# Performance work log

Hardware: AMD Instinct MI355X
Metric: run time of the kernel (lower is better)

Reference implementation:

```python
import jax, jax.numpy as jnp
import numpy as np
from jax import lax

B, N, D = 4, 4096, 1024
H, DH, K = 8, 128, 256  # heads, dim_head, linformer k
KERNEL = 32
PAD = (15, 16)  # torch padding='same' for even kernel: left=(k-1)//2, right=rest


def setup_inputs() -> dict:
    key = jax.random.key(0)
    ks = jax.random.split(key, 7)
    s = 0.02
    return {
        "x": jax.random.normal(ks[0], (B, N, D), dtype=jnp.float32),
        "Wq": jax.random.normal(ks[1], (D, D), dtype=jnp.float32) * s,
        "Wk": jax.random.normal(ks[2], (D, D), dtype=jnp.float32) * s,
        "Wpk": jax.random.normal(ks[3], (K, N, KERNEL), dtype=jnp.float32) * s,
        "bpk": jax.random.normal(ks[4], (K,), dtype=jnp.float32) * s,
        "Wo": jax.random.normal(ks[5], (D, D), dtype=jnp.float32) * s,
        "bo": jax.random.normal(ks[6], (D,), dtype=jnp.float32) * s,
    }


def reference(x, Wq, Wk, Wpk, bpk, Wo, bo):
    b, n, d = x.shape
    # linear projections (torch Linear: y = x @ W.T)
    q = x @ Wq.T                       # (b, n, h*dh)
    keys = x @ Wk.T                    # (b, n, h*dh)
    # Conv1d over feature length with seq positions as channels: (b, n, d) -> (b, k, d)
    keys = lax.conv_general_dilated(
        keys, Wpk, window_strides=(1,), padding=[PAD],
        dimension_numbers=("NCH", "OIH", "NCH"),
    ) + bpk[None, :, None]             # (b, K, h*dh)
    values = keys                      # share_kv=True
    # split heads
    q = q.reshape(b, n, H, DH).transpose(0, 2, 1, 3)        # (b, h, n, dh)
    kk = keys.reshape(b, K, H, DH).transpose(0, 2, 1, 3)    # (b, h, K, dh)
    vv = values.reshape(b, K, H, DH).transpose(0, 2, 1, 3)  # (b, h, K, dh)
    dots = jnp.einsum("bhnd,bhkd->bhnk", q, kk) * (DH ** -0.5)
    attn = jax.nn.softmax(dots, axis=-1)                    # dropout p=0.0 (eval)
    out = jnp.einsum("bhnk,bhkd->bhnd", attn, vv)
    out = out.transpose(0, 2, 1, 3).reshape(b, n, H * DH)
    return out @ Wo.T + bo
```

## Files before the change

kernel.cpp:

```cpp
#include <hip/hip_runtime.h>


typedef short v8s __attribute__((ext_vector_type(8)));
typedef float v4f __attribute__((ext_vector_type(4)));

#define MFMA16(a, b, c) __builtin_amdgcn_mfma_f32_16x16x32_bf16((a), (b), (c), 0, 0, 0)
#define WAITV(N) asm volatile("s_waitcnt vmcnt(" #N ")" ::: "memory")
#define SBAR() __builtin_amdgcn_s_barrier()

__device__ __forceinline__ unsigned short f2bf(float f) {
  unsigned int u = __float_as_uint(f);
  u += 0x7fffu + ((u >> 16) & 1u);
  return (unsigned short)(u >> 16);
}

__device__ __forceinline__ v8s cvt8(float4 a, float4 b) {
  v8s v;
  v[0] = (short)f2bf(a.x); v[1] = (short)f2bf(a.y);
  v[2] = (short)f2bf(a.z); v[3] = (short)f2bf(a.w);
  v[4] = (short)f2bf(b.x); v[5] = (short)f2bf(b.y);
  v[6] = (short)f2bf(b.z); v[7] = (short)f2bf(b.w);
  return v;
}

__device__ __forceinline__ void gld16(void* lds, const void* g) {
  __builtin_amdgcn_global_load_lds(
      (const __attribute__((address_space(1))) void*)g,
      (__attribute__((address_space(3))) void*)lds, 16, 0, 0);
}

__device__ __forceinline__ const v8s* frag_ptr(const short* base, int row, int g) {
  return (const v8s*)(base + row * 32 + (((g ^ (row >> 1)) & 3) << 3));
}

__global__ __launch_bounds__(256) void k_cvt(const float* __restrict__ src,
                                             short* __restrict__ dst, int n8) {
  const int i = blockIdx.x * 256 + threadIdx.x;
  if (i >= n8) return;
  const float4* s = (const float4*)src;
  ((v8s*)dst)[i] = cvt8(s[2 * i], s[2 * i + 1]);
}

__global__ __launch_bounds__(256) void k_reorder_wpk(const float* __restrict__ Wpk,
                                                     short* __restrict__ Wr) {
  __shared__ short T[64][40];
  const int k  = blockIdx.x >> 6;
  const int n0 = (blockIdx.x & 63) << 6;
  const int tid = threadIdx.x;
  {
    const int i = tid >> 2, t0 = (tid & 3) << 3;
    const float* p = Wpk + ((size_t)k * 4096 + n0 + i) * 32 + t0;
    float4 a = *(const float4*)p, b = *(const float4*)(p + 4);
    *(v8s*)&T[i][t0] = cvt8(a, b);
  }
  __syncthreads();
  {
    const int t = tid >> 3, j0 = (tid & 7) << 3;
    v8s o;
#pragma unroll
    for (int q = 0; q < 8; ++q) o[q] = T[j0 + q][t];
    *(v8s*)(Wr + ((size_t)t * 256 + k) * 4096 + n0 + j0) = o;
  }
}

__global__ __launch_bounds__(256) void k_init_kc(const float* __restrict__ bpk,
                                                 float* __restrict__ Kc) {
  const int idx = (blockIdx.x * 256 + threadIdx.x) * 4;
  const float v = bpk[(idx >> 10) & 255];
  float4 f; f.x = v; f.y = v; f.z = v; f.w = v;
  *(float4*)(Kc + idx) = f;
}

__global__ __launch_bounds__(256) void k_zero_pad(short* __restrict__ KpTp) {
  const int idx = blockIdx.x * 256 + threadIdx.x;
  const int ridx = idx >> 9, col8 = idx & 511;
  const int b = ridx >> 5, rr = ridx & 31;
  const int row = (rr < 15) ? rr : 1039 + (rr - 15);
  v8s z = {0, 0, 0, 0, 0, 0, 0, 0};
  *(v8s*)(KpTp + ((size_t)b * 1056 + row) * 4096 + col8 * 8) = z;
}

__global__ __launch_bounds__(256) void k_gemm_qk_v3(const short* __restrict__ xbf,
                                                    const short* __restrict__ Wqk,
                                                    short* __restrict__ Qbf,
                                                    short* __restrict__ Kp) {
  __shared__ short As[2][128][32];
  __shared__ short Bs[2][128][32];
  const int tid = threadIdx.x, lane = tid & 63, w = tid >> 6;
  const int m0 = blockIdx.x * 128, j0 = blockIdx.y * 128;
  const int wr = (w >> 1) * 64, wc = (w & 1) * 64;
  const int l15 = lane & 15, g = lane >> 4;
  const int sr = lane >> 2, sseg = lane & 3;

  v4f acc[4][4];
#pragma unroll
  for (int i = 0; i < 4; ++i)
#pragma unroll
    for (int j = 0; j < 4; ++j) acc[i][j] = (v4f)0.0f;

  auto stage = [&](int buf, int k0) {
#pragma unroll
    for (int q0 = 0; q0 < 2; ++q0) {
      const int rblk = (w * 2 + q0) << 4, r = rblk + sr;
      const int co = ((sseg ^ (r >> 1)) & 3) << 3;
      gld16(&As[buf][rblk][0], xbf + (size_t)(m0 + r) * 1024 + k0 + co);
      gld16(&Bs[buf][rblk][0], Wqk + (size_t)(j0 + r) * 1024 + k0 + co);
    }
  };

  stage(0, 0);
#pragma unroll 1
  for (int p = 0, buf = 0; p < 32; ++p, buf ^= 1) {
    if (p + 1 < 32) stage(buf ^ 1, (p + 1) * 32);
    if (p < 31) { WAITV(4); } else { WAITV(0); }
    SBAR();
    v8s af[4], bf4[4];
#pragma unroll
    for (int mi = 0; mi < 4; ++mi)
      af[mi] = *frag_ptr(&As[buf][0][0], wr + mi * 16 + l15, g);
#pragma unroll
    for (int ni = 0; ni < 4; ++ni)
      bf4[ni] = *frag_ptr(&Bs[buf][0][0], wc + ni * 16 + l15, g);
#pragma unroll
    for (int ni = 0; ni < 4; ++ni)
#pragma unroll
      for (int mi = 0; mi < 4; ++mi)
        acc[mi][ni] = MFMA16(af[mi], bf4[ni], acc[mi][ni]);
    SBAR();
  }
  const int rbase = (lane >> 4) * 4;
#pragma unroll
  for (int mi = 0; mi < 4; ++mi)
#pragma unroll
    for (int ni = 0; ni < 4; ++ni) {
      const int col = j0 + wc + ni * 16 + l15;
      short* dst = (col < 1024) ? Qbf : Kp;
      const int cj = (col < 1024) ? col : col - 1024;
#pragma unroll
      for (int r = 0; r < 4; ++r) {
        const int row = m0 + wr + mi * 16 + rbase + r;
        dst[(size_t)row * 1024 + cj] = (short)f2bf(acc[mi][ni][r]);
      }
    }
}

__global__ __launch_bounds__(256) void k_transpose_pad(const short* __restrict__ src,
                                                       short* __restrict__ dst) {
  __shared__ short T[64][72];
  const int r0 = blockIdx.x * 64, c0 = blockIdx.y * 64, b = blockIdx.z;
  const int tid = threadIdx.x;
  {
    const int i = tid >> 2, q = (tid & 3) << 4;
    const short* ps = src + ((size_t)b * 4096 + r0 + i) * 1024 + c0 + q;
    *(v8s*)&T[i][q]     = *(const v8s*)ps;
    *(v8s*)&T[i][q + 8] = *(const v8s*)(ps + 8);
  }
  __syncthreads();
  {
    const int j = tid >> 2, p = (tid & 3) << 4;
    v8s o0, o1;
#pragma unroll
    for (int t = 0; t < 8; ++t) o0[t] = T[p + t][j];
#pragma unroll
    for (int t = 0; t < 8; ++t) o1[t] = T[p + 8 + t][j];
    short* pd = dst + ((size_t)b * 1056 + 15 + c0 + j) * 4096 + r0 + p;
    *(v8s*)pd = o0;
    *(v8s*)(pd + 8) = o1;
  }
}

__global__ __launch_bounds__(256) void k_conv_v3(const short* __restrict__ Wr,
                                                 const short* __restrict__ KpTp,
                                                 float* __restrict__ Kc) {
  __shared__ short As[3][2][128][32];
  __shared__ short Kt[2][160][32];
  const int L = blockIdx.x;
  const int xcd = L & 7, jj = L >> 3;
  const int slice = xcd + ((jj >> 5) << 3), win = jj & 31;
  const int mt = slice >> 3, ns = slice & 7, nt = win >> 2, b = win & 3;
  const int K0 = mt * 128, D0 = nt * 128;
  const int tid = threadIdx.x, lane = tid & 63, w = tid >> 6;
  const int wr = (w >> 1) * 64, wc = (w & 1) * 64;
  const int l15 = lane & 15, g = lane >> 4;
  const int sr = lane >> 2, sseg = lane & 3;
  const short* KpTb = KpTp + (size_t)b * 1056 * 4096;

  v4f acc[4][4];
#pragma unroll
  for (int i = 0; i < 4; ++i)
#pragma unroll
    for (int j = 0; j < 4; ++j) acc[i][j] = (v4f)0.0f;

  auto stageAs = [&](int buf, int ph) {
    const int n0 = ns * 512 + (ph >> 4) * 32, t0 = (ph & 15) * 2;
#pragma unroll
    for (int q0 = 0; q0 < 4; ++q0) {
      const int q = w + q0 * 4;
      const int pl = q >> 3, rblk = (q & 7) << 4, r = rblk + sr;
      gld16(&As[buf][pl][rblk][0],
            Wr + ((size_t)(t0 + pl) * 256 + K0 + r) * 4096 + n0 +
                (((sseg ^ (r >> 1)) & 3) << 3));
    }
  };
  auto stageKt = [&](int buf, int nc) {
    const int n0 = ns * 512 + nc * 32;
    for (int q = w; q < 10; q += 4) {
      const int rblk = q << 4, r = rblk + sr;
      gld16(&Kt[buf][rblk][0],
            KpTb + (size_t)(D0 + r) * 4096 + n0 + (((sseg ^ (r >> 1)) & 3) << 3));
    }
  };

  stageKt(0, 0);
  stageAs(0, 0);
  stageAs(1, 1);
  int kb = 0;
#pragma unroll 1
  for (int p = 0; p < 256; ++p) {
    const int tp = p & 15;
    if (p + 2 < 256) {
      stageAs((p + 2) % 3, p + 2);
      if (tp == 14) stageKt(kb ^ 1, (p + 2) >> 4);
    }
    if (p < 254) { WAITV(8); } else if (p == 254) { WAITV(4); } else { WAITV(0); }
    SBAR();
    const short* Ab = &As[p % 3][0][0][0];
#pragma unroll
    for (int pl = 0; pl < 2; ++pl) {
      const int t = tp * 2 + pl;
      v8s af[4], bf4[4];
#pragma unroll
      for (int mi = 0; mi < 4; ++mi)
        af[mi] = *frag_ptr(Ab + pl * 128 * 32, wr + mi * 16 + l15, g);
#pragma unroll
      for (int ni = 0; ni < 4; ++ni)
        bf4[ni] = *frag_ptr(&Kt[kb][0][0], wc + ni * 16 + l15 + t, g);
#pragma unroll
      for (int ni = 0; ni < 4; ++ni)
#pragma unroll
        for (int mi = 0; mi < 4; ++mi)
          acc[mi][ni] = MFMA16(af[mi], bf4[ni], acc[mi][ni]);
    }
    SBAR();
    if (tp == 15) kb ^= 1;
  }

  float* kcb = Kc + (size_t)b * 256 * 1024;
  const int rbase = (lane >> 4) * 4;
#pragma unroll
  for (int mi = 0; mi < 4; ++mi)
#pragma unroll
    for (int ni = 0; ni < 4; ++ni)
#pragma unroll
      for (int r = 0; r < 4; ++r)
        atomicAdd(kcb + (size_t)(K0 + wr + mi * 16 + rbase + r) * 1024 +
                      (D0 + wc + ni * 16 + l15),
                  acc[mi][ni][r]);
}

__global__ __launch_bounds__(256) void k_kc_post(const float* __restrict__ Kc,
                                                 short* __restrict__ Kcbf,
                                                 short* __restrict__ KcT) {
  __shared__ short T[64][72];
  const int k0 = blockIdx.x * 64, d0 = blockIdx.y * 64, b = blockIdx.z;
  const int tid = threadIdx.x;
  {
    const int i = tid >> 2, q = (tid & 3) << 4;
    const float* ps = Kc + (size_t)(b * 256 + k0 + i) * 1024 + d0 + q;
    float4 f0 = *(const float4*)ps,       f1 = *(const float4*)(ps + 4);
    float4 f2 = *(const float4*)(ps + 8), f3 = *(const float4*)(ps + 12);
    v8s v0 = cvt8(f0, f1), v1 = cvt8(f2, f3);
    *(v8s*)&T[i][q] = v0;
    *(v8s*)&T[i][q + 8] = v1;
    short* pc = Kcbf + (size_t)(b * 256 + k0 + i) * 1024 + d0 + q;
    *(v8s*)pc = v0;
    *(v8s*)(pc + 8) = v1;
  }
  __syncthreads();
  {
    const int j = tid >> 2, p = (tid & 3) << 4;
    v8s o0, o1;
#pragma unroll
    for (int t = 0; t < 8; ++t) o0[t] = T[p + t][j];
#pragma unroll
    for (int t = 0; t < 8; ++t) o1[t] = T[p + 8 + t][j];
    short* pd = KcT + (size_t)(b * 1024 + d0 + j) * 256 + k0 + p;
    *(v8s*)pd = o0;
    *(v8s*)(pd + 8) = o1;
  }
}

__global__ __launch_bounds__(256) void k_attn(const short* __restrict__ Qbf,
                                              const short* __restrict__ Kcbf,
                                              const short* __restrict__ KcT,
                                              short* __restrict__ AO) {
  __shared__ short P[4][16][264];
  const int nt = blockIdx.x, h = blockIdx.y, b = blockIdx.z;
  const int tid = threadIdx.x, lane = tid & 63, w = tid >> 6;
  const int l15 = lane & 15, lg4 = (lane >> 4) * 4, lg8 = (lane >> 4) * 8;
  const float scale = 0.08838834764831845f;
  const size_t qb  = (size_t)b * 4096 * 1024 + (size_t)h * 128;
  const size_t kb  = (size_t)b * 256 * 1024 + (size_t)h * 128;
  const size_t vtb = ((size_t)b * 1024 + (size_t)h * 128) * 256;
  short (*Pw)[264] = P[w];
  const int n_wave = nt * 128 + w * 32;

#pragma unroll 1
  for (int half = 0; half < 2; ++half) {
    const int nbase = n_wave + half * 16;
    v8s aq[4];
#pragma unroll
    for (int kt = 0; kt < 4; ++kt)
      aq[kt] = *(const v8s*)(Qbf + qb + (size_t)(nbase + l15) * 1024 + kt * 32 + lg8);

    v4f dacc[16];
#pragma unroll
    for (int ct = 0; ct < 16; ++ct) dacc[ct] = (v4f)0.0f;
#pragma unroll 1
    for (int kt = 0; kt < 4; ++kt) {
#pragma unroll
      for (int ct = 0; ct < 16; ++ct) {
        v8s bk = *(const v8s*)(Kcbf + kb + (size_t)(ct * 16 + l15) * 1024 + kt * 32 + lg8);
        dacc[ct] = MFMA16(aq[kt], bk, dacc[ct]);
      }
    }
#pragma unroll
    for (int ct = 0; ct < 16; ++ct) dacc[ct] = dacc[ct] * scale;
    v4f m4 = dacc[0];
#pragma unroll
    for (int ct = 1; ct < 16; ++ct)
#pragma unroll
      for (int r = 0; r < 4; ++r) m4[r] = fmaxf(m4[r], dacc[ct][r]);
#pragma unroll
    for (int off = 1; off < 16; off <<= 1)
#pragma unroll
      for (int r = 0; r < 4; ++r) m4[r] = fmaxf(m4[r], __shfl_xor(m4[r], off, 64));
    v4f ssum = (v4f)0.0f;
#pragma unroll
    for (int ct = 0; ct < 16; ++ct)
#pragma unroll
      for (int r = 0; r < 4; ++r) {
        const float e = __expf(dacc[ct][r] - m4[r]);
        ssum[r] += e;
        Pw[lg4 + r][ct * 16 + l15] = (short)f2bf(e);
      }
#pragma unroll
    for (int off = 1; off < 16; off <<= 1)
#pragma unroll
      for (int r = 0; r < 4; ++r) ssum[r] += __shfl_xor(ssum[r], off, 64);
    __syncthreads();

    v4f oacc[8];
#pragma unroll
    for (int ct = 0; ct < 8; ++ct) oacc[ct] = (v4f)0.0f;
#pragma unroll 1
    for (int kt2 = 0; kt2 < 8; ++kt2) {
      v8s pa = *(const v8s*)&Pw[l15][kt2 * 32 + lg8];
#pragma unroll
      for (int ct = 0; ct < 8; ++ct) {
        v8s bv = *(const v8s*)(KcT + vtb + (size_t)(ct * 16 + l15) * 256 + kt2 * 32 + lg8);
        oacc[ct] = MFMA16(pa, bv, oacc[ct]);
      }
    }
    v4f inv;
#pragma unroll
    for (int r = 0; r < 4; ++r) inv[r] = 1.0f / ssum[r];
#pragma unroll
    for (int ct = 0; ct < 8; ++ct)
#pragma unroll
      for (int r = 0; r < 4; ++r)
        AO[qb + (size_t)(nbase + lg4 + r) * 1024 + ct * 16 + l15] =
            (short)f2bf(oacc[ct][r] * inv[r]);
    __syncthreads();
  }
}

__global__ __launch_bounds__(256) void k_gemm_out_v3(const short* __restrict__ AO,
                                                     const short* __restrict__ Wobf,
                                                     const float* __restrict__ bo,
                                                     float* __restrict__ out) {
  __shared__ short As[2][128][32];
  __shared__ short Bs[2][128][32];
  const int tid = threadIdx.x, lane = tid & 63, w = tid >> 6;
  const int m0 = blockIdx.x * 128, j0 = blockIdx.y * 128;
  const int wr = (w >> 1) * 64, wc = (w & 1) * 64;
  const int l15 = lane & 15, g = lane >> 4;
  const int sr = lane >> 2, sseg = lane & 3;

  v4f acc[4][4];
#pragma unroll
  for (int i = 0; i < 4; ++i)
#pragma unroll
    for (int j = 0; j < 4; ++j) acc[i][j] = (v4f)0.0f;

  auto stage = [&](int buf, int k0) {
#pragma unroll
    for (int q0 = 0; q0 < 2; ++q0) {
      const int rblk = (w * 2 + q0) << 4, r = rblk + sr;
      const int co = ((sseg ^ (r >> 1)) & 3) << 3;
      gld16(&As[buf][rblk][0], AO + (size_t)(m0 + r) * 1024 + k0 + co);
      gld16(&Bs[buf][rblk][0], Wobf + (size_t)(j0 + r) * 1024 + k0 + co);
    }
  };

  stage(0, 0);
#pragma unroll 1
  for (int p = 0, buf = 0; p < 32; ++p, buf ^= 1) {
    if (p + 1 < 32) stage(buf ^ 1, (p + 1) * 32);
    if (p < 31) { WAITV(4); } else { WAITV(0); }
    SBAR();
    v8s af[4], bf4[4];
#pragma unroll
    for (int mi = 0; mi < 4; ++mi)
      af[mi] = *frag_ptr(&As[buf][0][0], wr + mi * 16 + l15, g);
#pragma unroll
    for (int ni = 0; ni < 4; ++ni)
      bf4[ni] = *frag_ptr(&Bs[buf][0][0], wc + ni * 16 + l15, g);
#pragma unroll
    for (int ni = 0; ni < 4; ++ni)
#pragma unroll
      for (int mi = 0; mi < 4; ++mi)
        acc[mi][ni] = MFMA16(af[mi], bf4[ni], acc[mi][ni]);
    SBAR();
  }
  const int rbase = (lane >> 4) * 4;
#pragma unroll
  for (int mi = 0; mi < 4; ++mi)
#pragma unroll
    for (int ni = 0; ni < 4; ++ni) {
      const int col = j0 + wc + ni * 16 + l15;
      const float bias = bo[col];
#pragma unroll
      for (int r = 0; r < 4; ++r) {
        const int row = m0 + wr + mi * 16 + rbase + r;
        out[(size_t)row * 1024 + col] = acc[mi][ni][r] + bias;
      }
    }
}

extern "C" void kernel_launch(void* const* d_in, const int* in_sizes, int n_in,
                              void* d_out, int out_size, void* d_ws, size_t ws_size,
                              hipStream_t stream) {
  const float* x   = (const float*)d_in[0];
  const float* Wq  = (const float*)d_in[1];
  const float* Wk  = (const float*)d_in[2];
  const float* Wpk = (const float*)d_in[3];
  const float* bpk = (const float*)d_in[4];
  const float* Wo  = (const float*)d_in[5];
  const float* bo  = (const float*)d_in[6];

  const size_t OFF_WR   = 0;
  const size_t OFF_XBF  = 67108864;
  const size_t OFF_WQK  = 100663296;
  const size_t OFF_KPTP = 67108864;
  const size_t OFF_KCBF = 67108864;
  const size_t OFF_KCT  = 69206016;
  const size_t OFF_WOBF = 101711872;
  const size_t OFF_QBF  = 104857600;
  const size_t OFF_KP   = 138412032;
  const size_t OFF_KC   = 171966464;
  const size_t NEED     = 176160768;
  if (ws_size < NEED) return;

  char* ws = (char*)d_ws;
  short* Wr   = (short*)(ws + OFF_WR);
  short* xbf  = (short*)(ws + OFF_XBF);
  short* Wqk  = (short*)(ws + OFF_WQK);
  short* KpTp = (short*)(ws + OFF_KPTP);
  short* Kcbf = (short*)(ws + OFF_KCBF);
  short* KcT  = (short*)(ws + OFF_KCT);
  short* Wobf = (short*)(ws + OFF_WOBF);
  short* Qbf  = (short*)(ws + OFF_QBF);
  short* Kp   = (short*)(ws + OFF_KP);
  float* Kc   = (float*)(ws + OFF_KC);
  short* AO   = Kp;
  float* outp = (float*)d_out;

  k_cvt<<<dim3(8192), dim3(256), 0, stream>>>(x, xbf, 16777216 / 8);
  k_cvt<<<dim3(512),  dim3(256), 0, stream>>>(Wq, Wqk, 1048576 / 8);
  k_cvt<<<dim3(512),  dim3(256), 0, stream>>>(Wk, Wqk + 1048576, 1048576 / 8);
  k_reorder_wpk<<<dim3(16384), dim3(256), 0, stream>>>(Wpk, Wr);
  k_init_kc<<<dim3(1024), dim3(256), 0, stream>>>(bpk, Kc);
  k_gemm_qk_v3<<<dim3(128, 16), dim3(256), 0, stream>>>(xbf, Wqk, Qbf, Kp);
  k_transpose_pad<<<dim3(64, 16, 4), dim3(256), 0, stream>>>(Kp, KpTp);
  k_cvt<<<dim3(512), dim3(256), 0, stream>>>(Wo, Wobf, 1048576 / 8);
  k_zero_pad<<<dim3(256), dim3(256), 0, stream>>>(KpTp);
  k_conv_v3<<<dim3(512), dim3(256), 0, stream>>>(Wr, KpTp, Kc);
  k_kc_post<<<dim3(4, 16, 4), dim3(256), 0, stream>>>(Kc, Kcbf, KcT);
  k_attn<<<dim3(32, 8, 4), dim3(256), 0, stream>>>(Qbf, Kcbf, KcT, AO);
  k_gemm_out_v3<<<dim3(128, 8), dim3(256), 0, stream>>>(AO, Wobf, bo, outp);
}
```

Baseline: 638.4 us.

## Rewrite conv as larger-tile split-N GEMM with partial buffers and reduction

The conv kernel now uses 512-thread blocks with a 256x256 output tile covering all K rows, split over 16 slices of the sequence dimension. Each block writes plain stores into per-slice partial buffers placed in the output buffer, which a new reduce kernel sums together with the bias. This replaces the float atomicAdd accumulation and the bias-init kernel, and raises reuse of the Wr and Kt shared-memory tiles. The cost is 64MB of partial-buffer traffic plus an extra reduction pass, and fewer blocks (256) to fill the GPU.

```diff
diff --git a/kernel.cpp b/kernel.cpp
--- a/kernel.cpp
+++ b/kernel.cpp
@@ -63,14 +63,6 @@
   }
 }
 
-__global__ __launch_bounds__(256) void k_init_kc(const float* __restrict__ bpk,
-                                                 float* __restrict__ Kc) {
-  const int idx = (blockIdx.x * 256 + threadIdx.x) * 4;
-  const float v = bpk[(idx >> 10) & 255];
-  float4 f; f.x = v; f.y = v; f.z = v; f.w = v;
-  *(float4*)(Kc + idx) = f;
-}
-
 __global__ __launch_bounds__(256) void k_zero_pad(short* __restrict__ KpTp) {
   const int idx = blockIdx.x * 256 + threadIdx.x;
   const int ridx = idx >> 9, col8 = idx & 511;
@@ -169,93 +161,123 @@
   }
 }
 
-__global__ __launch_bounds__(256) void k_conv_v3(const short* __restrict__ Wr,
-                                                 const short* __restrict__ KpTp,
-                                                 float* __restrict__ Kc) {
-  __shared__ short As[3][2][128][32];
-  __shared__ short Kt[2][160][32];
-  const int L = blockIdx.x;
-  const int xcd = L & 7, jj = L >> 3;
-  const int slice = xcd + ((jj >> 5) << 3), win = jj & 31;
-  const int mt = slice >> 3, ns = slice & 7, nt = win >> 2, b = win & 3;
-  const int K0 = mt * 128, D0 = nt * 128;
+__global__ __launch_bounds__(512, 2) void k_conv_v4(const short* __restrict__ Wr,
+                                                    const short* __restrict__ KpTp,
+                                                    float* __restrict__ Pq) {
+  __shared__ short A[3][256][32];
+  __shared__ short Kt[2][384][32];
+  const int bid = blockIdx.x;
+  const int ns = (bid & 7) | (((bid >> 7) & 1) << 3);
+  const int j  = (bid >> 3) & 15;
+  const int b = j >> 2, nt = j & 3;
+  const int D0 = nt * 256;
+  const int nbase = ns * 256;
   const int tid = threadIdx.x, lane = tid & 63, w = tid >> 6;
-  const int wr = (w >> 1) * 64, wc = (w & 1) * 64;
+  const int wm = (w >> 2) * 128, wn = (w & 3) * 64;
   const int l15 = lane & 15, g = lane >> 4;
-  const int sr = lane >> 2, sseg = lane & 3;
+  const int lr = lane >> 2, lseg = lane & 3;
   const short* KpTb = KpTp + (size_t)b * 1056 * 4096;
 
-  v4f acc[4][4];
-#pragma unroll
-  for (int i = 0; i < 4; ++i)
-#pragma unroll
-    for (int j = 0; j < 4; ++j) acc[i][j] = (v4f)0.0f;
-
-  auto stageAs = [&](int buf, int ph) {
-    const int n0 = ns * 512 + (ph >> 4) * 32, t0 = (ph & 15) * 2;
-#pragma unroll
-    for (int q0 = 0; q0 < 4; ++q0) {
-      const int q = w + q0 * 4;
-      const int pl = q >> 3, rblk = (q & 7) << 4, r = rblk + sr;
-      gld16(&As[buf][pl][rblk][0],
-            Wr + ((size_t)(t0 + pl) * 256 + K0 + r) * 4096 + n0 +
-                (((sseg ^ (r >> 1)) & 3) << 3));
-    }
+  v4f acc[8][4];
+#pragma unroll
+  for (int mi = 0; mi < 8; ++mi)
+#pragma unroll
+    for (int ni = 0; ni < 4; ++ni) acc[mi][ni] = (v4f)0.0f;
+
+  auto stageA = [&](int buf, int s2, int q) {
+    const int t2 = s2 & 31, c2 = s2 >> 5;
+    const int rblk = q * 128 + w * 16;
+    const int row = rblk + lr;
+    const int sg = ((lseg ^ (row >> 1)) & 3) << 3;
+    gld16(&A[buf][rblk][0],
+          Wr + ((size_t)t2 * 256 + row) * 4096 + nbase + c2 * 32 + sg);
   };
-  auto stageKt = [&](int buf, int nc) {
-    const int n0 = ns * 512 + nc * 32;
-    for (int q = w; q < 10; q += 4) {
-      const int rblk = q << 4, r = rblk + sr;
-      gld16(&Kt[buf][rblk][0],
-            KpTb + (size_t)(D0 + r) * 4096 + n0 + (((sseg ^ (r >> 1)) & 3) << 3));
-    }
+  auto stageKt = [&](int buf, int c1, int q) {
+    const int rblk = q * 128 + w * 16;
+    const int row = rblk + lr;
+    const int srow = row < 287 ? row : 286;
+    const int sg = ((lseg ^ (row >> 1)) & 3) << 3;
+    gld16(&Kt[buf][rblk][0],
+          KpTb + (size_t)(D0 + srow) * 4096 + nbase + c1 * 32 + sg);
   };
 
-  stageKt(0, 0);
-  stageAs(0, 0);
-  stageAs(1, 1);
-  int kb = 0;
+  stageA(0, 0, 0); stageA(0, 0, 1);
+  stageKt(0, 0, 0); stageKt(0, 0, 1); stageKt(0, 0, 2);
+  stageA(1, 1, 0); stageA(1, 1, 1);
+  WAITV(2);
+  SBAR();
+
+  int ab = 0, pab = 2;
 #pragma unroll 1
-  for (int p = 0; p < 256; ++p) {
-    const int tp = p & 15;
-    if (p + 2 < 256) {
-      stageAs((p + 2) % 3, p + 2);
-      if (tp == 14) stageKt(kb ^ 1, (p + 2) >> 4);
-    }
-    if (p < 254) { WAITV(8); } else if (p == 254) { WAITV(4); } else { WAITV(0); }
-    SBAR();
-    const short* Ab = &As[p % 3][0][0][0];
-#pragma unroll
-    for (int pl = 0; pl < 2; ++pl) {
-      const int t = tp * 2 + pl;
-      v8s af[4], bf4[4];
+  for (int s = 0; s < 256; ++s) {
+    const int t = s & 31, c = s >> 5;
+    const short* Abp = &A[ab][0][0];
+    const short* Ktp = &Kt[c & 1][0][0];
+    v8s bq[4], aq[4];
+#pragma unroll
+    for (int ni = 0; ni < 4; ++ni)
+      bq[ni] = *frag_ptr(Ktp, wn + ni * 16 + l15 + t, g);
+#pragma unroll
+    for (int mi = 0; mi < 4; ++mi)
+      aq[mi] = *frag_ptr(Abp, wm + mi * 16 + l15, g);
+    if (s + 2 < 256) stageA(pab, s + 2, 0);
+    SBAR();
+    __builtin_amdgcn_s_setprio(1);
+#pragma unroll
+    for (int ni = 0; ni < 4; ++ni)
 #pragma unroll
       for (int mi = 0; mi < 4; ++mi)
-        af[mi] = *frag_ptr(Ab + pl * 128 * 32, wr + mi * 16 + l15, g);
-#pragma unroll
-      for (int ni = 0; ni < 4; ++ni)
-        bf4[ni] = *frag_ptr(&Kt[kb][0][0], wc + ni * 16 + l15 + t, g);
-#pragma unroll
-      for (int ni = 0; ni < 4; ++ni)
-#pragma unroll
-        for (int mi = 0; mi < 4; ++mi)
-          acc[mi][ni] = MFMA16(af[mi], bf4[ni], acc[mi][ni]);
-    }
-    SBAR();
-    if (tp == 15) kb ^= 1;
-  }
-
-  float* kcb = Kc + (size_t)b * 256 * 1024;
-  const int rbase = (lane >> 4) * 4;
-#pragma unroll
-  for (int mi = 0; mi < 4; ++mi)
-#pragma unroll
-    for (int ni = 0; ni < 4; ++ni)
+        acc[mi][ni] = MFMA16(aq[mi], bq[ni], acc[mi][ni]);
+    __builtin_amdgcn_s_setprio(0);
+    SBAR();
+    v8s aq2[4];
+#pragma unroll
+    for (int mi = 0; mi < 4; ++mi)
+      aq2[mi] = *frag_ptr(Abp, wm + 64 + mi * 16 + l15, g);
+    const bool ktst = ((unsigned)(t - 24) <= 2u) && (c < 7);
+    if (s + 2 < 256) stageA(pab, s + 2, 1);
+    if (ktst) stageKt((c + 1) & 1, c + 1, t - 24);
+    SBAR();
+    __builtin_amdgcn_s_setprio(1);
+#pragma unroll
+    for (int ni = 0; ni < 4; ++ni)
+#pragma unroll
+      for (int mi = 0; mi < 4; ++mi)
+        acc[4 + mi][ni] = MFMA16(aq2[mi], bq[ni], acc[4 + mi][ni]);
+    __builtin_amdgcn_s_setprio(0);
+    if (s < 254) {
+      if (ktst) { WAITV(3); } else { WAITV(2); }
+    } else if (s == 254) {
+      WAITV(0);
+    }
+    SBAR();
+    pab = ab; ab = (ab == 2) ? 0 : ab + 1;
+  }
+
+  float* Pp = Pq + (size_t)(ns * 4 + b) * 262144;
+#pragma unroll
+  for (int mi = 0; mi < 8; ++mi)
+#pragma unroll
+    for (int ni = 0; ni < 4; ++ni) {
+      const int col = D0 + wn + ni * 16 + l15;
 #pragma unroll
       for (int r = 0; r < 4; ++r)
-        atomicAdd(kcb + (size_t)(K0 + wr + mi * 16 + rbase + r) * 1024 +
-                      (D0 + wc + ni * 16 + l15),
-                  acc[mi][ni][r]);
+        Pp[(size_t)(wm + mi * 16 + g * 4 + r) * 1024 + col] = acc[mi][ni][r];
+    }
+}
+
+__global__ __launch_bounds__(256) void k_reduce_kc(const float* __restrict__ P,
+                                                   const float* __restrict__ bpk,
+                                                   float* __restrict__ Kc) {
+  const int i = (blockIdx.x * 256 + threadIdx.x) * 4;
+  const float bias = bpk[(i >> 10) & 255];
+  float4 s; s.x = bias; s.y = bias; s.z = bias; s.w = bias;
+#pragma unroll
+  for (int ns = 0; ns < 16; ++ns) {
+    float4 v = *(const float4*)(P + (size_t)ns * 1048576 + i);
+    s.x += v.x; s.y += v.y; s.z += v.z; s.w += v.w;
+  }
+  *(float4*)(Kc + i) = s;
 }
 
 __global__ __launch_bounds__(256) void k_kc_post(const float* __restrict__ Kc,
@@ -474,18 +496,19 @@
   short* Kp   = (short*)(ws + OFF_KP);
   float* Kc   = (float*)(ws + OFF_KC);
   short* AO   = Kp;
+  float* Ppart = (float*)d_out;
   float* outp = (float*)d_out;
 
   k_cvt<<<dim3(8192), dim3(256), 0, stream>>>(x, xbf, 16777216 / 8);
   k_cvt<<<dim3(512),  dim3(256), 0, stream>>>(Wq, Wqk, 1048576 / 8);
   k_cvt<<<dim3(512),  dim3(256), 0, stream>>>(Wk, Wqk + 1048576, 1048576 / 8);
   k_reorder_wpk<<<dim3(16384), dim3(256), 0, stream>>>(Wpk, Wr);
-  k_init_kc<<<dim3(1024), dim3(256), 0, stream>>>(bpk, Kc);
   k_gemm_qk_v3<<<dim3(128, 16), dim3(256), 0, stream>>>(xbf, Wqk, Qbf, Kp);
   k_transpose_pad<<<dim3(64, 16, 4), dim3(256), 0, stream>>>(Kp, KpTp);
   k_cvt<<<dim3(512), dim3(256), 0, stream>>>(Wo, Wobf, 1048576 / 8);
   k_zero_pad<<<dim3(256), dim3(256), 0, stream>>>(KpTp);
-  k_conv_v3<<<dim3(512), dim3(256), 0, stream>>>(Wr, KpTp, Kc);
+  k_conv_v4<<<dim3(256), dim3(512), 0, stream>>>(Wr, KpTp, Ppart);
+  k_reduce_kc<<<dim3(1024), dim3(256), 0, stream>>>(Ppart, bpk, Kc);
   k_kc_post<<<dim3(4, 16, 4), dim3(256), 0, stream>>>(Kc, Kcbf, KcT);
   k_attn<<<dim3(32, 8, 4), dim3(256), 0, stream>>>(Qbf, Kcbf, KcT, AO);
   k_gemm_out_v3<<<dim3(128, 8), dim3(256), 0, stream>>>(AO, Wobf, bo, outp);
```

New measurement: 633.1 us. No clear change (-0.8%).
